# Kernel optimization log

Measured on AMD Instinct MI355X. Metric: run time of the kernel, lower is better.

## Reference

```python
import jax, jax.numpy as jnp
import numpy as np

KH, KW, STRIDE = 3, 3, 1

def setup_inputs() -> dict:
    key = jax.random.key(0)
    x = jax.random.normal(key, (32, 64, 64, 64), dtype=jnp.float32)  # [B, C, H, W]
    return {"x": x}

def unfold(x, Kh, Kw, stride):
    B, C, H, W = x.shape
    Ho = H - (Kh - 1)  # number of row positions (loop bound in original)
    Wo = W - (Kw - 1)
    # Gather all patches with a small fixed Kh*Kw loop (vectorized over B,C,Ho,Wo).
    # Original flattens each patch [C, Kh, Kw] -> C*Kh*Kw (channel-major),
    # and enumerates positions row-major (i outer, j inner).
    slabs = [x[:, :, i * stride:i * stride + Ho, j * stride:j * stride + Wo]
             for i in range(Kh) for j in range(Kw)]          # each [B, C, Ho, Wo]
    p = jnp.stack(slabs, axis=2)                              # [B, C, Kh*Kw, Ho, Wo]
    return p.reshape(B, C * Kh * Kw, Ho * Wo)                 # [B, C*Kh*Kw, L]

def reference(x):
    return unfold(x, KH, KW, STRIDE)
```

## Files before the change

### kernel.cpp

```cpp
#include <hip/hip_runtime.h>


#define B 32
#define C 64
#define H 64
#define W 64
#define KH 3
#define KW 3
#define HO 62
#define WO 62
#define L (HO * WO)
#define L4 (L / 4)
#define K (C * KH * KW)

__global__ __launch_bounds__(256) void unfold_kernel(
    const float* __restrict__ x, float* __restrict__ out) {
    const int idx4 = blockIdx.x * blockDim.x + threadIdx.x;
    const int k    = blockIdx.y;
    const int b    = blockIdx.z;
    if (idx4 >= L4) return;

    const int c = k / (KH * KW);
    const int p = k - c * (KH * KW);
    const int i = p / KW;
    const int j = p - i * KW;

    const int l0 = idx4 * 4;
    int ho = l0 / WO;
    int wo = l0 - ho * WO;

    const float* __restrict__ xrow = x + ((size_t)(b * C + c)) * (H * W) + (size_t)i * W + j;

    float4 v;
    float r[4];
#pragma unroll
    for (int q = 0; q < 4; ++q) {
        r[q] = xrow[ho * W + wo];
        ++wo;
        if (wo == WO) { wo = 0; ++ho; }
    }
    v.x = r[0]; v.y = r[1]; v.z = r[2]; v.w = r[3];

    float4* __restrict__ out4 = (float4*)out;
    out4[(size_t)(b * K + k) * L4 + idx4] = v;
}

extern "C" void kernel_launch(void* const* d_in, const int* in_sizes, int n_in,
                              void* d_out, int out_size, void* d_ws, size_t ws_size,
                              hipStream_t stream) {
    const float* x = (const float*)d_in[0];
    float* out = (float*)d_out;

    dim3 block(256, 1, 1);
    dim3 grid((L4 + 255) / 256, K, B);
    unfold_kernel<<<grid, block, 0, stream>>>(x, out);
}
```

Baseline: 341.3 us.

## Stage each channel plane in LDS and emit all nine patch slabs per block

Each block now loads one full 64x64 input plane into shared memory with float4 loads, using a padded swizzle to avoid bank conflicts, then writes all nine kernel-offset slabs for that (b,c) from LDS. This removes the ninefold redundant global/L2 reads of the input and the per-element unaligned scalar loads. In exchange the grid shrinks to 2048 blocks, each using about 17 KB of LDS and doing a long serial write loop, which lowers parallelism and occupancy on a store-bound kernel.

Measured after the change: 313.8 us. 8.1% less time.

```diff
diff --git a/kernel.cpp b/kernel.cpp
--- a/kernel.cpp
+++ b/kernel.cpp
@@ -5,44 +5,62 @@
 #define C 64
 #define H 64
 #define W 64
-#define KH 3
-#define KW 3
 #define HO 62
 #define WO 62
 #define L (HO * WO)
 #define L4 (L / 4)
-#define K (C * KH * KW)
+#define KK 9
+
+__device__ __forceinline__ int sw(int p) { return p + (p >> 5); }
 
 __global__ __launch_bounds__(256) void unfold_kernel(
     const float* __restrict__ x, float* __restrict__ out) {
-    const int idx4 = blockIdx.x * blockDim.x + threadIdx.x;
-    const int k    = blockIdx.y;
-    const int b    = blockIdx.z;
-    if (idx4 >= L4) return;
+    __shared__ float tile[H * W + (H * W) / 32];
 
-    const int c = k / (KH * KW);
-    const int p = k - c * (KH * KW);
-    const int i = p / KW;
-    const int j = p - i * KW;
+    const int c   = blockIdx.x;
+    const int b   = blockIdx.y;
+    const int tid = threadIdx.x;
 
-    const int l0 = idx4 * 4;
-    int ho = l0 / WO;
-    int wo = l0 - ho * WO;
+    const float4* __restrict__ src =
+        (const float4*)(x + (((size_t)(b * C + c)) << 12));
+#pragma unroll
+    for (int r = 0; r < 4; ++r) {
+        const int p4 = tid + r * 256;
+        float4 v = src[p4];
+        const int p = p4 * 4;
+        tile[sw(p)]     = v.x;
+        tile[sw(p + 1)] = v.y;
+        tile[sw(p + 2)] = v.z;
+        tile[sw(p + 3)] = v.w;
+    }
+    __syncthreads();
 
-    const float* __restrict__ xrow = x + ((size_t)(b * C + c)) * (H * W) + (size_t)i * W + j;
+    float4* __restrict__ dst =
+        (float4*)out + (size_t)(b * C + c) * KK * L4;
 
-    float4 v;
-    float r[4];
 #pragma unroll
-    for (int q = 0; q < 4; ++q) {
-        r[q] = xrow[ho * W + wo];
-        ++wo;
-        if (wo == WO) { wo = 0; ++ho; }
+    for (int k = 0; k < KK; ++k) {
+        const int i = k / 3;
+        const int j = k - i * 3;
+        const int base = i * W + j;
+        for (int t = tid; t < L4; t += 256) {
+            const int l0 = t * 4;
+            int ho = l0 / WO;
+            int wo = l0 - ho * WO;
+            int addr = base + ho * W + wo;
+            float r[4];
+#pragma unroll
+            for (int q = 0; q < 4; ++q) {
+                r[q] = tile[sw(addr)];
+                ++addr;
+                ++wo;
+                if (wo == WO) { wo = 0; addr += (W - WO); }
+            }
+            float4 v;
+            v.x = r[0]; v.y = r[1]; v.z = r[2]; v.w = r[3];
+            dst[k * L4 + t] = v;
+        }
     }
-    v.x = r[0]; v.y = r[1]; v.z = r[2]; v.w = r[3];
-
-    float4* __restrict__ out4 = (float4*)out;
-    out4[(size_t)(b * K + k) * L4 + idx4] = v;
 }
 
 extern "C" void kernel_launch(void* const* d_in, const int* in_sizes, int n_in,
@@ -52,6 +70,6 @@
     float* out = (float*)d_out;
 
     dim3 block(256, 1, 1);
-    dim3 grid((L4 + 255) / 256, K, B);
+    dim3 grid(C, B, 1);
     unfold_kernel<<<grid, block, 0, stream>>>(x, out);
 }
```
